# Performance work log

Measured on AMD Instinct MI355X. Metric: run time of the kernel, lower is better.

The kernel has to match this reference:

```python
import jax, jax.numpy as jnp
import numpy as np
from jax.ops import segment_sum

N_NODES = 100000


def setup_inputs() -> dict:
    key = jax.random.key(0)
    k1, k2, k3, k4, k5 = jax.random.split(key, 5)
    E = 3200000
    x = jax.random.normal(k1, (N_NODES, 8), dtype=jnp.float32)
    edge_index = jax.random.randint(k2, (2, E), 0, N_NODES, dtype=jnp.int64)
    edge_attr = jax.random.uniform(k3, (E,), dtype=jnp.float32)
    W = jax.random.normal(k4, (8, 64), dtype=jnp.float32) * (1.0 / np.sqrt(8.0))
    b = jax.random.normal(k5, (64,), dtype=jnp.float32) * 0.01
    return {"x": x, "edge_index": edge_index, "edge_attr": edge_attr, "W": W, "b": b}


def reference(x, edge_index, edge_attr, W, b):
    # GCNConv(8, 64) with symmetric normalization and self-loops (PyG defaults).
    N = x.shape[0]
    # Add self-loops with weight 1.0
    loops = jnp.arange(N, dtype=edge_index.dtype)
    row = jnp.concatenate([edge_index[0], loops])            # source nodes [E+N]
    col = jnp.concatenate([edge_index[1], loops])            # target nodes [E+N]
    ew = jnp.concatenate([edge_attr, jnp.ones((N,), dtype=edge_attr.dtype)])
    # Symmetric degree normalization: deg computed on target index
    deg = segment_sum(ew, col, num_segments=N)               # [N]
    dis = jnp.where(deg > 0, jax.lax.rsqrt(jnp.where(deg > 0, deg, 1.0)), 0.0)
    norm = dis[row] * ew * dis[col]                          # [E+N]
    # Linear transform first (in=8 -> out=64), then gather/scale/scatter-add
    xt = x @ W                                               # [N, 64]
    msgs = xt[row] * norm[:, None]                           # [E+N, 64]
    out = segment_sum(msgs, col, num_segments=N) + b         # [N, 64]
    return out
```

## Files before the change

### kernel.cpp

```cpp
#include <hip/hip_runtime.h>


#define NBMAX 1024
#define PSH   7
#define BINSZ 128
#define TILE  4096
#define EPT   4
#define CAP   6144

static inline size_t ws_align(size_t x) { return (x + 255) & ~(size_t)255; }

__global__ void init_k(const unsigned* w, unsigned* orw, unsigned* cnt, int E) {
    int t = threadIdx.x;
    for (int i = t; i < NBMAX; i += 256) cnt[i] = 0u;
    __shared__ unsigned s;
    if (t == 0) s = 0u;
    __syncthreads();
    unsigned v = 0;
    int lim = (E < 2048) ? E : 2048;
    for (int i = t; i < lim; i += 256)
        v |= w[2 * i + 1];
    atomicOr(&s, v);
    __syncthreads();
    if (t == 0) *orw = s;
}

__global__ void hist_k(const void* ei, const unsigned* orw, unsigned* cnt,
                       int E, int NB) {
    __shared__ unsigned lh[NBMAX];
    const bool is64 = (*orw == 0u);
    const int* e32 = (const int*)ei;
    const long long* e64 = (const long long*)ei;
    for (int i = threadIdx.x; i < NB; i += blockDim.x) lh[i] = 0u;
    __syncthreads();
    int t = blockIdx.x * blockDim.x + threadIdx.x;
    int st = gridDim.x * blockDim.x;
    for (int e = t; e < E; e += st) {
        int c = is64 ? (int)e64[E + e] : e32[E + e];
        atomicAdd(&lh[c >> PSH], 1u);
    }
    __syncthreads();
    for (int i = threadIdx.x; i < NB; i += blockDim.x) {
        unsigned v = lh[i];
        if (v) atomicAdd(&cnt[i], v);
    }
}

__global__ void scan_k(const unsigned* cnt, unsigned* offs, unsigned* gcur, int NB) {
    __shared__ unsigned sc[NBMAX];
    int t = threadIdx.x;
    unsigned v0 = (t < NB) ? cnt[t] : 0u;
    sc[t] = v0;
    __syncthreads();
    for (int d = 1; d < 1024; d <<= 1) {
        unsigned v = (t >= d) ? sc[t - d] : 0u;
        __syncthreads();
        sc[t] += v;
        __syncthreads();
    }
    unsigned excl = sc[t] - v0;
    if (t < NB) { offs[t] = excl; gcur[t] = excl; }
    if (t == 0) offs[NB] = sc[NB - 1];
}

__global__ __launch_bounds__(1024)
void scat_k(const void* ei, const float* ea, const unsigned* orw,
            unsigned* gcur, unsigned long long* pay, int E, int NB, int ntiles) {
    __shared__ unsigned long long lp[TILE];
    __shared__ unsigned short lbin[TILE];
    __shared__ unsigned lh[NBMAX];
    __shared__ unsigned lo[NBMAX + 1];
    __shared__ unsigned gb[NBMAX];
    const bool is64 = (*orw == 0u);
    const int* e32 = (const int*)ei;
    const long long* e64 = (const long long*)ei;
    const int t = threadIdx.x;

    for (int tile = blockIdx.x; tile < ntiles; tile += gridDim.x) {
        int base = tile * TILE;
        int tc = E - base; if (tc > TILE) tc = TILE;

        for (int i = t; i < NB; i += 1024) lh[i] = 0u;
        __syncthreads();

        int bn[EPT]; unsigned rk[EPT]; unsigned long long pv[EPT];
        #pragma unroll
        for (int i = 0; i < EPT; ++i) {
            int e = base + i * 1024 + t;
            bn[i] = -1;
            if (e < base + tc) {
                int c, r;
                if (is64) { c = (int)e64[E + e]; r = (int)e64[e]; }
                else      { c = e32[E + e];      r = e32[e]; }
                float w = ea[e];
                bn[i] = c >> PSH;
                pv[i] = ((unsigned long long)__float_as_uint(w) << 32)
                        | ((unsigned)r << 8) | (unsigned)(c & (BINSZ - 1));
                rk[i] = atomicAdd(&lh[bn[i]], 1u);
            }
        }
        __syncthreads();

        unsigned v0 = (t < NB) ? lh[t] : 0u;
        lo[t] = v0;
        __syncthreads();
        for (int d = 1; d < 1024; d <<= 1) {
            unsigned v = (t >= d) ? lo[t - d] : 0u;
            __syncthreads();
            lo[t] += v;
            __syncthreads();
        }
        unsigned excl = lo[t] - v0;
        if (t < NB && v0) gb[t] = atomicAdd(&gcur[t], v0);
        if (t < NB) lo[t] = excl;
        if (t == 0) lo[NB] = (unsigned)tc;
        __syncthreads();

        #pragma unroll
        for (int i = 0; i < EPT; ++i)
            if (bn[i] >= 0) {
                unsigned pos = lo[bn[i]] + rk[i];
                lp[pos] = pv[i];
                lbin[pos] = (unsigned short)bn[i];
            }
        __syncthreads();

        for (int s = t; s < tc; s += 1024) {
            int a = lbin[s];
            pay[(size_t)gb[a] + (unsigned)s - lo[a]] = lp[s];
        }
        __syncthreads();
    }
}

__global__ __launch_bounds__(1024)
void sort2_k(const unsigned long long* pay, const unsigned* offs,
             unsigned long long* pay2, unsigned* noffs, float* dis,
             const float* x, float* y, int N, int E) {
    __shared__ unsigned long long lp[CAP];
    __shared__ unsigned cnt[BINSZ];
    __shared__ unsigned loc[BINSZ];
    __shared__ unsigned cur[BINSZ];
    __shared__ float dw[BINSZ];
    __shared__ float sdis[BINSZ];
    int b = blockIdx.x, t = threadIdx.x;
    if (t < BINSZ) { cnt[t] = 0u; dw[t] = 0.f; }
    if (b == 0 && t == 0) noffs[N] = (unsigned)E;
    __syncthreads();
    unsigned base = offs[b], len = offs[b + 1] - base;
    for (unsigned j = t; j < len; j += 1024) {
        unsigned long long p = pay[base + j];
        unsigned lc = (unsigned)p & 255u;
        atomicAdd(&cnt[lc], 1u);
        atomicAdd(&dw[lc], __uint_as_float((unsigned)(p >> 32)));
    }
    __syncthreads();
    if (t < BINSZ) loc[t] = cnt[t];
    __syncthreads();
    for (int d = 1; d < BINSZ; d <<= 1) {
        unsigned v = 0;
        if (t < BINSZ && t >= d) v = loc[t - d];
        __syncthreads();
        if (t < BINSZ && t >= d) loc[t] += v;
        __syncthreads();
    }
    if (t < BINSZ) {
        unsigned excl = loc[t] - cnt[t];
        cur[t] = excl;
        int node = b * BINSZ + t;
        float dval = 0.f;
        if (node < N) {
            noffs[node] = base + excl;
            float d = 1.0f + dw[t];
            dval = (d > 0.f) ? rsqrtf(d) : 0.f;
            dis[node] = dval;
        }
        sdis[t] = dval;
    }
    __syncthreads();
    for (unsigned j = t; j < len; j += 1024) {
        unsigned long long p = pay[base + j];
        unsigned lc = (unsigned)p & 255u;
        unsigned pos = atomicAdd(&cur[lc], 1u);
        if (pos < CAP) lp[pos] = p;
        else pay2[(size_t)base + pos] = p;
    }
    __syncthreads();
    unsigned m = len < CAP ? len : CAP;
    for (unsigned j = t; j < m; j += 1024)
        pay2[(size_t)base + j] = lp[j];
    int gbase = b * (BINSZ * 8);
    int gi = gbase + t;
    if (t < BINSZ * 8 && gi < N * 8)
        y[gi] = sdis[t >> 3] * x[gi];
}

__global__ __launch_bounds__(256)
void agg_k(const unsigned long long* pay2, const unsigned* noffs,
           const float* dis, const float* y, const float* Wm, const float* bv,
           float* out, int N) {
    __shared__ float ag[4][8];
    const float4* y4 = (const float4*)y;
    int t = threadIdx.x;
    int wv = t >> 6, lane = t & 63;
    int slot = lane >> 1, h = lane & 1;
    int node = blockIdx.x * 4 + wv;
    float wr[8];
    #pragma unroll
    for (int k = 0; k < 8; ++k) wr[k] = Wm[k * 64 + lane];
    float o2 = bv[lane];
    float a0 = 0.f, a1 = 0.f, a2 = 0.f, a3 = 0.f;
    if (node < N) {
        unsigned s = noffs[node], e = noffs[node + 1];
        for (unsigned j = s + slot; j < e; j += 32) {
            unsigned long long p = pay2[j];
            unsigned r = ((unsigned)p >> 8) & 0xFFFFFFu;
            float ew = __uint_as_float((unsigned)(p >> 32));
            float4 v = y4[(size_t)r * 2 + h];
            a0 += ew * v.x; a1 += ew * v.y; a2 += ew * v.z; a3 += ew * v.w;
        }
    }
    #pragma unroll
    for (int m = 2; m <= 32; m <<= 1) {
        a0 += __shfl_xor(a0, m);
        a1 += __shfl_xor(a1, m);
        a2 += __shfl_xor(a2, m);
        a3 += __shfl_xor(a3, m);
    }
    if (node < N && slot == 0) {
        float dc = dis[node];
        float4 vy = y4[(size_t)node * 2 + h];
        ag[wv][h * 4 + 0] = dc * (a0 + vy.x);
        ag[wv][h * 4 + 1] = dc * (a1 + vy.y);
        ag[wv][h * 4 + 2] = dc * (a2 + vy.z);
        ag[wv][h * 4 + 3] = dc * (a3 + vy.w);
    }
    __syncthreads();
    if (node < N) {
        #pragma unroll
        for (int k = 0; k < 8; ++k) o2 += ag[wv][k] * wr[k];
        out[(size_t)node * 64 + lane] = o2;
    }
}

__global__ void fb_init_k(float* deg, float4* agg4, int N) {
    int i = blockIdx.x * blockDim.x + threadIdx.x, st = gridDim.x * blockDim.x;
    for (; i < N; i += st) {
        deg[i] = 1.0f;
        agg4[2 * i] = make_float4(0.f, 0.f, 0.f, 0.f);
        agg4[2 * i + 1] = make_float4(0.f, 0.f, 0.f, 0.f);
    }
}
__global__ void fb_deg_k(const void* ei, const float* ea, const unsigned* orw,
                         float* deg, int E) {
    const bool is64 = (*orw == 0u);
    const int* e32 = (const int*)ei;
    const long long* e64 = (const long long*)ei;
    int e = blockIdx.x * blockDim.x + threadIdx.x, st = gridDim.x * blockDim.x;
    for (; e < E; e += st) {
        int c = is64 ? (int)e64[E + e] : e32[E + e];
        atomicAdd(&deg[c], ea[e]);
    }
}
__global__ void fb_dis_k(float* deg, int N) {
    int i = blockIdx.x * blockDim.x + threadIdx.x, st = gridDim.x * blockDim.x;
    for (; i < N; i += st) {
        float d = deg[i];
        deg[i] = (d > 0.f) ? rsqrtf(d) : 0.f;
    }
}
__global__ void fb_edge_k(const void* ei, const float* ea, const unsigned* orw,
                          const float* dis, const float* x, float* agg, int E) {
    const bool is64 = (*orw == 0u);
    const int* e32 = (const int*)ei;
    const long long* e64 = (const long long*)ei;
    int e = blockIdx.x * blockDim.x + threadIdx.x, st = gridDim.x * blockDim.x;
    for (; e < E; e += st) {
        int r, c;
        if (is64) { r = (int)e64[e]; c = (int)e64[E + e]; }
        else      { r = e32[e];      c = e32[E + e]; }
        float nrm = dis[r] * ea[e] * dis[c];
        const float4* xr = (const float4*)(x + (size_t)r * 8);
        float4 a = xr[0], bb = xr[1];
        float* ag = agg + (size_t)c * 8;
        atomicAdd(ag + 0, nrm * a.x);  atomicAdd(ag + 1, nrm * a.y);
        atomicAdd(ag + 2, nrm * a.z);  atomicAdd(ag + 3, nrm * a.w);
        atomicAdd(ag + 4, nrm * bb.x); atomicAdd(ag + 5, nrm * bb.y);
        atomicAdd(ag + 6, nrm * bb.z); atomicAdd(ag + 7, nrm * bb.w);
    }
}
__global__ void fb_out_k(const float* x, const float* Wm, const float* bv,
                         const float* dis, const float* agg, float* out, int N) {
    int lane = threadIdx.x & 63;
    int wid = blockIdx.x * (blockDim.x >> 6) + (threadIdx.x >> 6);
    int nw = gridDim.x * (blockDim.x >> 6);
    float wr[8];
    #pragma unroll
    for (int k = 0; k < 8; ++k) wr[k] = Wm[k * 64 + lane];
    float bj = bv[lane];
    for (int i = wid; i < N; i += nw) {
        float d = dis[i];
        float ink = 0.f;
        if (lane < 8) ink = agg[(size_t)i * 8 + lane] + d * d * x[(size_t)i * 8 + lane];
        float acc = bj;
        #pragma unroll
        for (int k = 0; k < 8; ++k) acc += __shfl(ink, k) * wr[k];
        out[(size_t)i * 64 + lane] = acc;
    }
}

extern "C" void kernel_launch(void* const* d_in, const int* in_sizes, int n_in,
                              void* d_out, int out_size, void* d_ws, size_t ws_size,
                              hipStream_t stream) {
    const float* x  = (const float*)d_in[0];
    const void*  ei = d_in[1];
    const float* ea = (const float*)d_in[2];
    const float* Wm = (const float*)d_in[3];
    const float* bv = (const float*)d_in[4];
    float* out = (float*)d_out;

    const int N = in_sizes[0] / 8;
    const int E = in_sizes[2];
    const int NB = (N + BINSZ - 1) / BINSZ;

    char* ws = (char*)d_ws;
    size_t o = 0;
    unsigned* orw   = (unsigned*)(ws + o); o += 256;
    unsigned* cnt   = (unsigned*)(ws + o); o += ws_align(NBMAX * 4);
    unsigned* offs  = (unsigned*)(ws + o); o += ws_align((NBMAX + 1) * 4);
    unsigned* gcur  = (unsigned*)(ws + o); o += ws_align(NBMAX * 4);
    float* dis      = (float*)(ws + o);    o += ws_align((size_t)N * 4);
    unsigned* noffs = (unsigned*)(ws + o); o += ws_align((size_t)(N + 1) * 4);
    float* y        = (float*)(ws + o);    o += ws_align((size_t)N * 8 * 4);
    unsigned long long* pay = (unsigned long long*)(ws + o);
    o += ws_align((size_t)E * 8);
    unsigned long long* pay2 = (unsigned long long*)(ws + o);
    o += ws_align((size_t)E * 8);

    const int ntiles = (E + TILE - 1) / TILE;

    if (NB <= NBMAX && E >= 2048 && o <= ws_size) {
        init_k<<<1, 256, 0, stream>>>((const unsigned*)ei, orw, cnt, E);
        hist_k<<<256, 512, 0, stream>>>(ei, orw, cnt, E, NB);
        scan_k<<<1, 1024, 0, stream>>>(cnt, offs, gcur, NB);
        scat_k<<<ntiles, 1024, 0, stream>>>(ei, ea, orw, gcur, pay, E, NB, ntiles);
        sort2_k<<<NB, 1024, 0, stream>>>(pay, offs, pay2, noffs, dis, x, y, N, E);
        agg_k<<<(N + 3) / 4, 256, 0, stream>>>(pay2, noffs, dis, y, Wm, bv, out, N);
    } else {
        float* agg = (float*)(ws + 256 + ws_align((size_t)N * 4));
        init_k<<<1, 256, 0, stream>>>((const unsigned*)ei, orw, cnt, E);
        fb_init_k<<<(N + 255) / 256, 256, 0, stream>>>(dis, (float4*)agg, N);
        fb_deg_k<<<2048, 256, 0, stream>>>(ei, ea, orw, dis, E);
        fb_dis_k<<<(N + 255) / 256, 256, 0, stream>>>(dis, N);
        fb_edge_k<<<2048, 256, 0, stream>>>(ei, ea, orw, dis, x, agg, E);
        fb_out_k<<<2048, 256, 0, stream>>>(x, Wm, bv, dis, agg, out, N);
    }
}
```

Baseline: 129.1 us.

## Fuse per-bin local sort with aggregation and use wave-shuffle scans

Splits the old sort2 kernel into a node-stats kernel (degree, dis, y) and a fused kernel that re-buckets each bin's edges in shared memory and aggregates directly from LDS. This removes the pay2 global buffer round-trip. Overflowing edges beyond the LDS capacity are accumulated with shared atomics instead. Block-wide Hillis-Steele scans are replaced by wavefront shuffle scans, and the scatter tile grows to 6144 edges per block. In exchange, pay is read twice and each bin's aggregation runs in a single block with 16 waves covering 128 nodes.

```diff
diff --git a/kernel.cpp b/kernel.cpp
--- a/kernel.cpp
+++ b/kernel.cpp
@@ -4,8 +4,8 @@
 #define NBMAX 1024
 #define PSH   7
 #define BINSZ 128
-#define TILE  4096
-#define EPT   4
+#define TILE  6144
+#define EPT   6
 #define CAP   6144
 
 static inline size_t ws_align(size_t x) { return (x + 255) & ~(size_t)255; }
@@ -47,20 +47,30 @@
 }
 
 __global__ void scan_k(const unsigned* cnt, unsigned* offs, unsigned* gcur, int NB) {
-    __shared__ unsigned sc[NBMAX];
-    int t = threadIdx.x;
+    __shared__ unsigned wsum[16];
+    int t = threadIdx.x, lane = t & 63, wv = t >> 6;
     unsigned v0 = (t < NB) ? cnt[t] : 0u;
-    sc[t] = v0;
-    __syncthreads();
-    for (int d = 1; d < 1024; d <<= 1) {
-        unsigned v = (t >= d) ? sc[t - d] : 0u;
-        __syncthreads();
-        sc[t] += v;
-        __syncthreads();
-    }
-    unsigned excl = sc[t] - v0;
+    unsigned s = v0;
+    #pragma unroll
+    for (int d = 1; d < 64; d <<= 1) {
+        unsigned u = __shfl_up(s, d);
+        if (lane >= d) s += u;
+    }
+    if (lane == 63) wsum[wv] = s;
+    __syncthreads();
+    if (t < 16) {
+        unsigned w = wsum[t];
+        #pragma unroll
+        for (int d = 1; d < 16; d <<= 1) {
+            unsigned u = __shfl_up(w, d, 16);
+            if (t >= d) w += u;
+        }
+        wsum[t] = w;
+    }
+    __syncthreads();
+    unsigned excl = s - v0 + (wv ? wsum[wv - 1] : 0u);
     if (t < NB) { offs[t] = excl; gcur[t] = excl; }
-    if (t == 0) offs[NB] = sc[NB - 1];
+    if (t == NB - 1) offs[NB] = excl + v0;
 }
 
 __global__ __launch_bounds__(1024)
@@ -69,12 +79,13 @@
     __shared__ unsigned long long lp[TILE];
     __shared__ unsigned short lbin[TILE];
     __shared__ unsigned lh[NBMAX];
-    __shared__ unsigned lo[NBMAX + 1];
+    __shared__ unsigned lo[NBMAX];
     __shared__ unsigned gb[NBMAX];
+    __shared__ unsigned wsum[16];
     const bool is64 = (*orw == 0u);
     const int* e32 = (const int*)ei;
     const long long* e64 = (const long long*)ei;
-    const int t = threadIdx.x;
+    const int t = threadIdx.x, lane = t & 63, wv = t >> 6;
 
     for (int tile = blockIdx.x; tile < ntiles; tile += gridDim.x) {
         int base = tile * TILE;
@@ -102,18 +113,29 @@
         __syncthreads();
 
         unsigned v0 = (t < NB) ? lh[t] : 0u;
-        lo[t] = v0;
-        __syncthreads();
-        for (int d = 1; d < 1024; d <<= 1) {
-            unsigned v = (t >= d) ? lo[t - d] : 0u;
-            __syncthreads();
-            lo[t] += v;
-            __syncthreads();
-        }
-        unsigned excl = lo[t] - v0;
-        if (t < NB && v0) gb[t] = atomicAdd(&gcur[t], v0);
-        if (t < NB) lo[t] = excl;
-        if (t == 0) lo[NB] = (unsigned)tc;
+        unsigned s = v0;
+        #pragma unroll
+        for (int d = 1; d < 64; d <<= 1) {
+            unsigned u = __shfl_up(s, d);
+            if (lane >= d) s += u;
+        }
+        if (lane == 63) wsum[wv] = s;
+        __syncthreads();
+        if (t < 16) {
+            unsigned w = wsum[t];
+            #pragma unroll
+            for (int d = 1; d < 16; d <<= 1) {
+                unsigned u = __shfl_up(w, d, 16);
+                if (t >= d) w += u;
+            }
+            wsum[t] = w;
+        }
+        __syncthreads();
+        unsigned excl = s - v0 + (wv ? wsum[wv - 1] : 0u);
+        if (t < NB) {
+            lo[t] = excl;
+            if (v0) gb[t] = atomicAdd(&gcur[t], v0);
+        }
         __syncthreads();
 
         #pragma unroll
@@ -125,25 +147,23 @@
             }
         __syncthreads();
 
-        for (int s = t; s < tc; s += 1024) {
-            int a = lbin[s];
-            pay[(size_t)gb[a] + (unsigned)s - lo[a]] = lp[s];
+        for (int q = t; q < tc; q += 1024) {
+            int a = lbin[q];
+            pay[(size_t)gb[a] + (unsigned)q - lo[a]] = lp[q];
         }
         __syncthreads();
     }
 }
 
 __global__ __launch_bounds__(1024)
-void sort2_k(const unsigned long long* pay, const unsigned* offs,
-             unsigned long long* pay2, unsigned* noffs, float* dis,
-             const float* x, float* y, int N, int E) {
-    __shared__ unsigned long long lp[CAP];
+void nodestat_k(const unsigned long long* pay, const unsigned* offs,
+                unsigned* noffs, float* dis, const float* x, float* y,
+                int N, int E) {
     __shared__ unsigned cnt[BINSZ];
-    __shared__ unsigned loc[BINSZ];
-    __shared__ unsigned cur[BINSZ];
     __shared__ float dw[BINSZ];
     __shared__ float sdis[BINSZ];
-    int b = blockIdx.x, t = threadIdx.x;
+    __shared__ unsigned wpart[2];
+    int b = blockIdx.x, t = threadIdx.x, lane = t & 63, wv = t >> 6;
     if (t < BINSZ) { cnt[t] = 0u; dw[t] = 0.f; }
     if (b == 0 && t == 0) noffs[N] = (unsigned)E;
     __syncthreads();
@@ -155,18 +175,17 @@
         atomicAdd(&dw[lc], __uint_as_float((unsigned)(p >> 32)));
     }
     __syncthreads();
-    if (t < BINSZ) loc[t] = cnt[t];
-    __syncthreads();
-    for (int d = 1; d < BINSZ; d <<= 1) {
-        unsigned v = 0;
-        if (t < BINSZ && t >= d) v = loc[t - d];
-        __syncthreads();
-        if (t < BINSZ && t >= d) loc[t] += v;
-        __syncthreads();
-    }
+    unsigned v0 = (t < BINSZ) ? cnt[t] : 0u;
+    unsigned s = v0;
+    #pragma unroll
+    for (int d = 1; d < 64; d <<= 1) {
+        unsigned u = __shfl_up(s, d);
+        if (lane >= d) s += u;
+    }
+    if (t < BINSZ && lane == 63) wpart[wv] = s;
+    __syncthreads();
     if (t < BINSZ) {
-        unsigned excl = loc[t] - cnt[t];
-        cur[t] = excl;
+        unsigned excl = s - v0 + (wv == 1 ? wpart[0] : 0u);
         int node = b * BINSZ + t;
         float dval = 0.f;
         if (node < N) {
@@ -178,68 +197,90 @@
         sdis[t] = dval;
     }
     __syncthreads();
+    int gi = b * (BINSZ * 8) + t;
+    if (gi < N * 8) y[gi] = sdis[t >> 3] * x[gi];
+}
+
+__global__ __launch_bounds__(1024)
+void aggfuse_k(const unsigned long long* pay, const unsigned* offs,
+               const unsigned* noffs, const float* dis, const float* y,
+               const float* Wm, const float* bv, float* out, int N) {
+    __shared__ unsigned long long lp[CAP];
+    __shared__ float spill[BINSZ][8];
+    __shared__ unsigned loc[BINSZ];
+    __shared__ unsigned cur[BINSZ];
+    const float4* y4 = (const float4*)y;
+    int b = blockIdx.x, t = threadIdx.x, lane = t & 63, wv = t >> 6;
+    unsigned base = offs[b], len = offs[b + 1] - base;
+    ((float*)spill)[t] = 0.f;
+    if (t < BINSZ) {
+        int node = b * BINSZ + t;
+        unsigned l = (node < N) ? (noffs[node] - base) : len;
+        loc[t] = l; cur[t] = l;
+    }
+    __syncthreads();
     for (unsigned j = t; j < len; j += 1024) {
         unsigned long long p = pay[base + j];
         unsigned lc = (unsigned)p & 255u;
         unsigned pos = atomicAdd(&cur[lc], 1u);
         if (pos < CAP) lp[pos] = p;
-        else pay2[(size_t)base + pos] = p;
-    }
-    __syncthreads();
-    unsigned m = len < CAP ? len : CAP;
-    for (unsigned j = t; j < m; j += 1024)
-        pay2[(size_t)base + j] = lp[j];
-    int gbase = b * (BINSZ * 8);
-    int gi = gbase + t;
-    if (t < BINSZ * 8 && gi < N * 8)
-        y[gi] = sdis[t >> 3] * x[gi];
-}
-
-__global__ __launch_bounds__(256)
-void agg_k(const unsigned long long* pay2, const unsigned* noffs,
-           const float* dis, const float* y, const float* Wm, const float* bv,
-           float* out, int N) {
-    __shared__ float ag[4][8];
-    const float4* y4 = (const float4*)y;
-    int t = threadIdx.x;
-    int wv = t >> 6, lane = t & 63;
-    int slot = lane >> 1, h = lane & 1;
-    int node = blockIdx.x * 4 + wv;
+        else {
+            unsigned r = ((unsigned)p >> 8) & 0xFFFFFFu;
+            float ew = __uint_as_float((unsigned)(p >> 32));
+            float4 u = y4[(size_t)r * 2], v = y4[(size_t)r * 2 + 1];
+            atomicAdd(&spill[lc][0], ew * u.x); atomicAdd(&spill[lc][1], ew * u.y);
+            atomicAdd(&spill[lc][2], ew * u.z); atomicAdd(&spill[lc][3], ew * u.w);
+            atomicAdd(&spill[lc][4], ew * v.x); atomicAdd(&spill[lc][5], ew * v.y);
+            atomicAdd(&spill[lc][6], ew * v.z); atomicAdd(&spill[lc][7], ew * v.w);
+        }
+    }
+    __syncthreads();
     float wr[8];
     #pragma unroll
     for (int k = 0; k < 8; ++k) wr[k] = Wm[k * 64 + lane];
-    float o2 = bv[lane];
-    float a0 = 0.f, a1 = 0.f, a2 = 0.f, a3 = 0.f;
-    if (node < N) {
-        unsigned s = noffs[node], e = noffs[node + 1];
-        for (unsigned j = s + slot; j < e; j += 32) {
-            unsigned long long p = pay2[j];
-            unsigned r = ((unsigned)p >> 8) & 0xFFFFFFu;
-            float ew = __uint_as_float((unsigned)(p >> 32));
-            float4 v = y4[(size_t)r * 2 + h];
-            a0 += ew * v.x; a1 += ew * v.y; a2 += ew * v.z; a3 += ew * v.w;
-        }
-    }
-    #pragma unroll
-    for (int m = 2; m <= 32; m <<= 1) {
-        a0 += __shfl_xor(a0, m);
-        a1 += __shfl_xor(a1, m);
-        a2 += __shfl_xor(a2, m);
-        a3 += __shfl_xor(a3, m);
-    }
-    if (node < N && slot == 0) {
-        float dc = dis[node];
-        float4 vy = y4[(size_t)node * 2 + h];
-        ag[wv][h * 4 + 0] = dc * (a0 + vy.x);
-        ag[wv][h * 4 + 1] = dc * (a1 + vy.y);
-        ag[wv][h * 4 + 2] = dc * (a2 + vy.z);
-        ag[wv][h * 4 + 3] = dc * (a3 + vy.w);
-    }
-    __syncthreads();
-    if (node < N) {
-        #pragma unroll
-        for (int k = 0; k < 8; ++k) o2 += ag[wv][k] * wr[k];
-        out[(size_t)node * 64 + lane] = o2;
+    float bj = bv[lane];
+    int slot = lane >> 1, h = lane & 1;
+    for (int i = 0; i < 8; ++i) {
+        int ln = wv + (i << 4);
+        int node = b * BINSZ + ln;
+        float a0 = 0.f, a1 = 0.f, a2 = 0.f, a3 = 0.f;
+        if (node < N) {
+            unsigned s = loc[ln];
+            unsigned e = (ln < BINSZ - 1) ? loc[ln + 1] : len;
+            unsigned eL = e < CAP ? e : CAP;
+            for (unsigned j = s + slot; j < eL; j += 32) {
+                unsigned long long p = lp[j];
+                unsigned r = ((unsigned)p >> 8) & 0xFFFFFFu;
+                float ew = __uint_as_float((unsigned)(p >> 32));
+                float4 v = y4[(size_t)r * 2 + h];
+                a0 += ew * v.x; a1 += ew * v.y; a2 += ew * v.z; a3 += ew * v.w;
+            }
+        }
+        #pragma unroll
+        for (int m = 2; m <= 32; m <<= 1) {
+            a0 += __shfl_xor(a0, m);
+            a1 += __shfl_xor(a1, m);
+            a2 += __shfl_xor(a2, m);
+            a3 += __shfl_xor(a3, m);
+        }
+        float r0 = 0.f, r1 = 0.f, r2 = 0.f, r3 = 0.f;
+        if (slot == 0 && node < N) {
+            float dc = dis[node];
+            float4 vy = y4[(size_t)node * 2 + h];
+            r0 = dc * (a0 + spill[ln][h * 4 + 0] + vy.x);
+            r1 = dc * (a1 + spill[ln][h * 4 + 1] + vy.y);
+            r2 = dc * (a2 + spill[ln][h * 4 + 2] + vy.z);
+            r3 = dc * (a3 + spill[ln][h * 4 + 3] + vy.w);
+        }
+        float g0 = __shfl(r0, 0), g1 = __shfl(r1, 0);
+        float g2 = __shfl(r2, 0), g3 = __shfl(r3, 0);
+        float g4 = __shfl(r0, 1), g5 = __shfl(r1, 1);
+        float g6 = __shfl(r2, 1), g7 = __shfl(r3, 1);
+        if (node < N) {
+            float o = bj + g0 * wr[0] + g1 * wr[1] + g2 * wr[2] + g3 * wr[3]
+                         + g4 * wr[4] + g5 * wr[5] + g6 * wr[6] + g7 * wr[7];
+            out[(size_t)node * 64 + lane] = o;
+        }
     }
 }
 
@@ -334,8 +375,6 @@
     float* y        = (float*)(ws + o);    o += ws_align((size_t)N * 8 * 4);
     unsigned long long* pay = (unsigned long long*)(ws + o);
     o += ws_align((size_t)E * 8);
-    unsigned long long* pay2 = (unsigned long long*)(ws + o);
-    o += ws_align((size_t)E * 8);
 
     const int ntiles = (E + TILE - 1) / TILE;
 
@@ -344,8 +383,8 @@
         hist_k<<<256, 512, 0, stream>>>(ei, orw, cnt, E, NB);
         scan_k<<<1, 1024, 0, stream>>>(cnt, offs, gcur, NB);
         scat_k<<<ntiles, 1024, 0, stream>>>(ei, ea, orw, gcur, pay, E, NB, ntiles);
-        sort2_k<<<NB, 1024, 0, stream>>>(pay, offs, pay2, noffs, dis, x, y, N, E);
-        agg_k<<<(N + 3) / 4, 256, 0, stream>>>(pay2, noffs, dis, y, Wm, bv, out, N);
+        nodestat_k<<<NB, 1024, 0, stream>>>(pay, offs, noffs, dis, x, y, N, E);
+        aggfuse_k<<<NB, 1024, 0, stream>>>(pay, offs, noffs, dis, y, Wm, bv, out, N);
     } else {
         float* agg = (float*)(ws + 256 + ws_align((size_t)N * 4));
         init_k<<<1, 256, 0, stream>>>((const unsigned*)ei, orw, cnt, E);
```

Result: no change. 128.3 us (-0.6%).
